# Performance work log

Measured on AMD Instinct MI355X. Metric: run time of the kernel, lower is better.

The kernel has to match this reference:

```python
import jax, jax.numpy as jnp
import numpy as np

N = 12288
E = 393216
D_IN, D_HID, D_OUT = 128, 128, 64


def gcn_conv(x, edge_index, W, b, num_nodes):
    # PyG GCNConv: h = x @ W; add self-loops; sym-normalize; scatter-add; + b
    h = x @ W  # [N, F]
    row, col = edge_index[0], edge_index[1]
    sl = jnp.arange(num_nodes, dtype=edge_index.dtype)
    row = jnp.concatenate([row, sl])
    col = jnp.concatenate([col, sl])
    deg = jax.ops.segment_sum(jnp.ones_like(col, dtype=h.dtype), col, num_segments=num_nodes)
    dinv = jax.lax.rsqrt(jnp.maximum(deg, 1e-12))
    norm = dinv[row] * dinv[col]  # [E+N]
    msgs = h[row] * norm[:, None]
    out = jax.ops.segment_sum(msgs, col, num_segments=num_nodes)
    return out + b


def setup_inputs() -> dict:
    key = jax.random.key(0)
    k1, k2, k3, k4, k5 = jax.random.split(key, 5)
    x = jax.random.uniform(k1, (N, D_IN), dtype=jnp.float32)
    edge_index = jax.random.randint(k2, (2, E), 0, N, dtype=jnp.int64)
    # Glorot-style init for GCN weights, zeros for biases (PyG defaults)
    W1 = jax.random.normal(k3, (D_IN, D_HID), dtype=jnp.float32) * (1.0 / np.sqrt(D_IN))
    b1 = jnp.zeros((D_HID,), dtype=jnp.float32)
    W2 = jax.random.normal(k4, (D_HID, D_OUT), dtype=jnp.float32) * (1.0 / np.sqrt(D_HID))
    b2 = jnp.zeros((D_OUT,), dtype=jnp.float32)
    return {"x": x, "edge_index": edge_index, "W1": W1, "b1": b1, "W2": W2, "b2": b2}


def reference(x, edge_index, W1, b1, W2, b2):
    h = jax.nn.relu(gcn_conv(x, edge_index, W1, b1, N))
    latent = gcn_conv(h, edge_index, W2, b2, N)  # [N, D_OUT]
    return latent @ latent.T  # [N, N] gram-matrix decoder
```

## Files before the change

### kernel.cpp

```cpp
#include <hip/hip_runtime.h>

#define NN   12288
#define EE   393216
#define DIN  128
#define DHID 128
#define DOUT 64
#define CAP  96

typedef __attribute__((ext_vector_type(8))) short bf16x8;
typedef __attribute__((ext_vector_type(4))) float f32x4;
typedef __attribute__((ext_vector_type(4))) short s16x4;

__device__ __forceinline__ short f2bf(float f) {
    unsigned u = __float_as_uint(f);
    unsigned r = (u + 0x7fffu + ((u >> 16) & 1u)) >> 16;
    return (short)r;
}
__device__ __forceinline__ float bf2f(short h) {
    return __uint_as_float(((unsigned)(unsigned short)h) << 16);
}

#define GEMM1_BLOCKS 768
#define FILL_BLOCKS  512
__global__ __launch_bounds__(256) void k_fill_gemm1(const float* __restrict__ x,
                                                    const int* __restrict__ row,
                                                    const int* __restrict__ col,
                                                    const float* __restrict__ W1,
                                                    unsigned* __restrict__ cursor,
                                                    int* __restrict__ bucket,
                                                    float* __restrict__ g1) {
    const int b = blockIdx.x, t = threadIdx.x;
    if (b < GEMM1_BLOCKS) {
        __shared__ float xs[16 * DIN];
        const int r0 = b * 16;
        for (int j = t; j < 16 * DIN; j += 256) xs[j] = x[(size_t)r0 * DIN + j];
        __syncthreads();
        const int c = t & 127, rg = (t >> 7) * 8;
        float acc[8] = {};
        for (int k = 0; k < DIN; ++k) {
            float w = W1[k * DHID + c];
#pragma unroll
            for (int r = 0; r < 8; ++r) acc[r] += xs[(rg + r) * DIN + k] * w;
        }
#pragma unroll
        for (int r = 0; r < 8; ++r) g1[(size_t)(r0 + rg + r) * DHID + c] = acc[r];
    } else {
        const int gid = (b - GEMM1_BLOCKS) * 256 + t;
#pragma unroll
        for (int q = 0; q < 3; ++q) {
            int e = gid + q * (FILL_BLOCKS * 256);
            int c = col[e];
            unsigned p = atomicAdd(&cursor[c], 1u);
            if (p < CAP) bucket[(size_t)c * CAP + p] = row[e];
        }
    }
}

__global__ __launch_bounds__(256) void k_gather1_gemm2(const float* __restrict__ g1,
                                                       const int* __restrict__ bucket,
                                                       const unsigned* __restrict__ cursor,
                                                       const float* __restrict__ b1,
                                                       const float* __restrict__ W2,
                                                       float* __restrict__ g2) {
    __shared__ float hs[4][DHID];
    const int lane = threadIdx.x & 63, wave = threadIdx.x >> 6;
    const int c = blockIdx.x * 4 + wave;
    const unsigned cnt = cursor[c];
    const float dc = rsqrtf((float)cnt + 1.0f);
    const unsigned e = cnt < CAP ? cnt : CAP;
    const f32x4* __restrict__ G4 = (const f32x4*)g1;
    const int* __restrict__ bk = bucket + (size_t)c * CAP;
    const int sub = lane >> 5, col4 = lane & 31;

    f32x4 acc = (f32x4){0.f, 0.f, 0.f, 0.f};
    if (sub == 0) acc = G4[(size_t)c * 32 + col4] * dc;

    unsigned i = 0;
    int pr[4];
    if (i + 8 <= e) {
#pragma unroll
        for (int p = 0; p < 4; ++p) pr[p] = bk[i + 2 * p + sub];
    }
    for (; i + 8 <= e;) {
        int r[4];
#pragma unroll
        for (int p = 0; p < 4; ++p) r[p] = pr[p];
        const unsigned ni = i + 8;
        if (ni + 8 <= e) {
#pragma unroll
            for (int p = 0; p < 4; ++p) pr[p] = bk[ni + 2 * p + sub];
        }
        float d[4];
        f32x4 v[4];
#pragma unroll
        for (int p = 0; p < 4; ++p) {
            d[p] = rsqrtf((float)cursor[r[p]] + 1.0f);
            v[p] = G4[(size_t)r[p] * 32 + col4];
        }
#pragma unroll
        for (int p = 0; p < 4; ++p) acc += v[p] * d[p];
        i = ni;
    }
    for (; i + 2 <= e; i += 2) {
        int rr = bk[i + sub];
        float d = rsqrtf((float)cursor[rr] + 1.0f);
        acc += G4[(size_t)rr * 32 + col4] * d;
    }
    if (i < e && sub == 0) {
        int rr = bk[i];
        float d = rsqrtf((float)cursor[rr] + 1.0f);
        acc += G4[(size_t)rr * 32 + col4] * d;
    }
    acc.x += __shfl_xor(acc.x, 32);
    acc.y += __shfl_xor(acc.y, 32);
    acc.z += __shfl_xor(acc.z, 32);
    acc.w += __shfl_xor(acc.w, 32);

    f32x4 bb = ((const f32x4*)b1)[col4];
    f32x4 o = acc * dc + bb;
    o.x = fmaxf(o.x, 0.f);
    o.y = fmaxf(o.y, 0.f);
    o.z = fmaxf(o.z, 0.f);
    o.w = fmaxf(o.w, 0.f);
    if (sub == 0) ((f32x4*)hs[wave])[col4] = o;

    float a2 = 0.f;
#pragma unroll 8
    for (int k = 0; k < DHID; ++k) a2 += hs[wave][k] * W2[k * DOUT + lane];
    g2[(size_t)c * DOUT + lane] = a2 * dc;
}

__global__ __launch_bounds__(256) void k_gather2(const float* __restrict__ g2,
                                                 const int* __restrict__ bucket,
                                                 const unsigned* __restrict__ cursor,
                                                 const float* __restrict__ b2,
                                                 short* __restrict__ H,
                                                 short* __restrict__ Lo) {
    const int lane = threadIdx.x & 63, wave = threadIdx.x >> 6;
    const int c = blockIdx.x * 4 + wave;
    const unsigned cnt = cursor[c];
    const float dc = rsqrtf((float)cnt + 1.0f);
    const unsigned e = cnt < CAP ? cnt : CAP;
    const f32x4* __restrict__ G4 = (const f32x4*)g2;
    const int* __restrict__ bk = bucket + (size_t)c * CAP;
    const int sub = lane >> 4, col4 = lane & 15;

    f32x4 acc = (f32x4){0.f, 0.f, 0.f, 0.f};
    if (sub == 0) acc = G4[(size_t)c * 16 + col4];

    unsigned i = 0;
    int pr0 = 0, pr1 = 0;
    if (i + 8 <= e) { pr0 = bk[i + sub]; pr1 = bk[i + 4 + sub]; }
    for (; i + 8 <= e;) {
        int r0 = pr0, r1 = pr1;
        const unsigned ni = i + 8;
        if (ni + 8 <= e) { pr0 = bk[ni + sub]; pr1 = bk[ni + 4 + sub]; }
        f32x4 v0 = G4[(size_t)r0 * 16 + col4];
        f32x4 v1 = G4[(size_t)r1 * 16 + col4];
        acc += v0;
        acc += v1;
        i = ni;
    }
    for (; i + 4 <= e; i += 4) {
        int rr = bk[i + sub];
        acc += G4[(size_t)rr * 16 + col4];
    }
    if (i < e) {
        if (sub < (int)(e - i)) {
            int rr = bk[i + sub];
            acc += G4[(size_t)rr * 16 + col4];
        }
    }
    acc.x += __shfl_xor(acc.x, 16); acc.x += __shfl_xor(acc.x, 32);
    acc.y += __shfl_xor(acc.y, 16); acc.y += __shfl_xor(acc.y, 32);
    acc.z += __shfl_xor(acc.z, 16); acc.z += __shfl_xor(acc.z, 32);
    acc.w += __shfl_xor(acc.w, 16); acc.w += __shfl_xor(acc.w, 32);

    if (sub == 0) {
        f32x4 bb = ((const f32x4*)b2)[col4];
        f32x4 v = acc * dc + bb;
        s16x4 h4, l4;
        h4.x = f2bf(v.x); l4.x = f2bf(v.x - bf2f(h4.x));
        h4.y = f2bf(v.y); l4.y = f2bf(v.y - bf2f(h4.y));
        h4.z = f2bf(v.z); l4.z = f2bf(v.z - bf2f(h4.z));
        h4.w = f2bf(v.w); l4.w = f2bf(v.w - bf2f(h4.w));
        ((s16x4*)H)[(size_t)c * 16 + col4] = h4;
        ((s16x4*)Lo)[(size_t)c * 16 + col4] = l4;
    }
}

#define NTILE 96
#define NPAIR ((NTILE * (NTILE + 1)) / 2)
__global__ __launch_bounds__(256) void k_gram(const short* __restrict__ H,
                                              const short* __restrict__ L,
                                              float* __restrict__ out) {
    __shared__ float P[64][132];
    const int tid  = threadIdx.x;
    const int lane = tid & 63;
    const int wave = tid >> 6;

    const int Lb = blockIdx.x;
    int bi = (int)((193.0f - sqrtf(193.0f * 193.0f - 8.0f * (float)Lb)) * 0.5f);
    if (bi < 0) bi = 0;
    if (bi > NTILE - 1) bi = NTILE - 1;
    while (bi * NTILE - (bi * (bi - 1)) / 2 > Lb) --bi;
    while ((bi + 1) * NTILE - ((bi + 1) * bi) / 2 <= Lb) ++bi;
    const int bj = bi + (Lb - (bi * NTILE - (bi * (bi - 1)) / 2));

    const int wm = wave >> 1, wn = wave & 1;
    const int row0 = bi * 128 + wm * 64;
    const int col0 = bj * 128 + wn * 64;
    const int fr = lane & 15;
    const int fk = (lane >> 4) << 3;
    const int crow = (lane >> 4) * 4;
    const bool mirror = (bi != bj);

    bf16x8 aH[4][2], aL[4][2];
#pragma unroll
    for (int m = 0; m < 4; ++m)
#pragma unroll
        for (int k = 0; k < 2; ++k) {
            size_t off = (size_t)(row0 + m * 16 + fr) * DOUT + k * 32 + fk;
            aH[m][k] = *(const bf16x8*)(H + off);
            aL[m][k] = *(const bf16x8*)(L + off);
        }

    f32x4 acc[4][4];
#pragma unroll
    for (int n = 0; n < 4; ++n)
#pragma unroll
        for (int m = 0; m < 4; ++m) acc[n][m] = (f32x4){0.f, 0.f, 0.f, 0.f};

#pragma unroll
    for (int n = 0; n < 4; ++n) {
        bf16x8 bH[2], bL[2];
#pragma unroll
        for (int k = 0; k < 2; ++k) {
            size_t off = (size_t)(col0 + n * 16 + fr) * DOUT + k * 32 + fk;
            bH[k] = *(const bf16x8*)(H + off);
            bL[k] = *(const bf16x8*)(L + off);
        }
#pragma unroll
        for (int m = 0; m < 4; ++m)
#pragma unroll
            for (int k = 0; k < 2; ++k) {
                acc[n][m] = __builtin_amdgcn_mfma_f32_16x16x32_bf16(aL[m][k], bH[k], acc[n][m], 0, 0, 0);
                acc[n][m] = __builtin_amdgcn_mfma_f32_16x16x32_bf16(aH[m][k], bL[k], acc[n][m], 0, 0, 0);
                acc[n][m] = __builtin_amdgcn_mfma_f32_16x16x32_bf16(aH[m][k], bH[k], acc[n][m], 0, 0, 0);
            }
    }

    const size_t gr0 = (size_t)bi * 128, gc0 = (size_t)bj * 128;
#pragma unroll
    for (int h = 0; h < 2; ++h) {
        __syncthreads();
        if (wm == h) {
#pragma unroll
            for (int n = 0; n < 4; ++n)
#pragma unroll
                for (int m = 0; m < 4; ++m)
#pragma unroll
                    for (int j = 0; j < 4; ++j)
                        P[m * 16 + crow + j][wn * 64 + n * 16 + fr] = acc[n][m][j];
        }
        __syncthreads();
#pragma unroll
        for (int it = 0; it < 8; ++it) {
            int idx = it * 256 + tid;
            int r = idx >> 5, c4 = (idx & 31) << 2;
            f32x4 v = *(const f32x4*)&P[r][c4];
            __builtin_nontemporal_store(v, (f32x4*)&out[(gr0 + h * 64 + r) * NN + gc0 + c4]);
        }
        if (mirror) {
#pragma unroll
            for (int it = 0; it < 8; ++it) {
                int idx = it * 256 + tid;
                int r = idx >> 4, c4 = (idx & 15) << 2;
                f32x4 v;
                v.x = P[c4 + 0][r];
                v.y = P[c4 + 1][r];
                v.z = P[c4 + 2][r];
                v.w = P[c4 + 3][r];
                __builtin_nontemporal_store(v, (f32x4*)&out[(gc0 + r) * NN + gr0 + h * 64 + c4]);
            }
        }
    }
}

extern "C" void kernel_launch(void* const* d_in, const int* in_sizes, int n_in,
                              void* d_out, int out_size, void* d_ws, size_t ws_size,
                              hipStream_t stream) {
    const float* x  = (const float*)d_in[0];
    const int*   ei = (const int*)d_in[1];
    const float* W1 = (const float*)d_in[2];
    const float* b1 = (const float*)d_in[3];
    const float* W2 = (const float*)d_in[4];
    const float* b2 = (const float*)d_in[5];
    float* out = (float*)d_out;

    const int* row = ei;
    const int* col = ei + EE;

    char* w = (char*)d_ws;
    unsigned* cursor = (unsigned*)w; w += (size_t)NN * 4;
    int*      bucket = (int*)w;      w += (size_t)NN * CAP * 4;
    float*    g1     = (float*)w;    w += (size_t)NN * DHID * 4;
    float*    g2     = (float*)w;    w += (size_t)NN * DOUT * 4;
    short*    latH   = (short*)w;    w += (size_t)NN * DOUT * 2;
    short*    latL   = (short*)w;    w += (size_t)NN * DOUT * 2;

    hipMemsetAsync(cursor, 0, (size_t)NN * 4, stream);

    k_fill_gemm1<<<GEMM1_BLOCKS + FILL_BLOCKS, 256, 0, stream>>>(x, row, col, W1, cursor, bucket, g1);
    k_gather1_gemm2<<<NN / 4, 256, 0, stream>>>(g1, bucket, cursor, b1, W2, g2);
    k_gather2<<<NN / 4, 256, 0, stream>>>(g2, bucket, cursor, b2, latH, latL);

    k_gram<<<NPAIR, 256, 0, stream>>>(latH, latL, out);
}
```

Measured before the change: 207.9 us.

## Fuse memset, fill/GEMM1, gather1 and gather2 into one cooperative kernel

Replaces the memset plus three separate kernel launches with a single cooperative persistent kernel of 768 blocks that uses grid.sync between phases (cursor clear, bucket fill and GEMM1, gather1+GEMM2, gather2). Per-node gather code is factored into device helpers shared by the fallback kernels. The aim is to remove launch overhead and inter-kernel gaps. In exchange, the grid-wide barriers cost time, each block now serially handles 16 nodes per gather phase with lower occupancy, and the old kernels remain only as a fallback if the cooperative launch fails.

```diff
diff --git a/kernel.cpp b/kernel.cpp
--- a/kernel.cpp
+++ b/kernel.cpp
@@ -1,4 +1,7 @@
 #include <hip/hip_runtime.h>
+#include <hip/hip_cooperative_groups.h>
+
+namespace cg = cooperative_groups;
 
 #define NN   12288
 #define EE   393216
@@ -6,6 +9,7 @@
 #define DHID 128
 #define DOUT 64
 #define CAP  96
+#define NBC  768
 
 typedef __attribute__((ext_vector_type(8))) short bf16x8;
 typedef __attribute__((ext_vector_type(4))) float f32x4;
@@ -18,6 +22,190 @@
 }
 __device__ __forceinline__ float bf2f(short h) {
     return __uint_as_float(((unsigned)(unsigned short)h) << 16);
+}
+
+__device__ __forceinline__ void gather1_gemm2_node(int c, const float* __restrict__ g1,
+                                                   const int* __restrict__ bucket,
+                                                   const unsigned* __restrict__ cursor,
+                                                   const float* __restrict__ b1,
+                                                   const float* __restrict__ W2,
+                                                   float* __restrict__ g2,
+                                                   float* __restrict__ hrow,
+                                                   int lane) {
+    const unsigned cnt = cursor[c];
+    const float dc = rsqrtf((float)cnt + 1.0f);
+    const unsigned e = cnt < CAP ? cnt : CAP;
+    const f32x4* __restrict__ G4 = (const f32x4*)g1;
+    const int* __restrict__ bk = bucket + (size_t)c * CAP;
+    const int sub = lane >> 5, col4 = lane & 31;
+
+    f32x4 acc = (f32x4){0.f, 0.f, 0.f, 0.f};
+    if (sub == 0) acc = G4[(size_t)c * 32 + col4] * dc;
+
+    unsigned i = 0;
+    int pr[4];
+    if (i + 8 <= e) {
+#pragma unroll
+        for (int p = 0; p < 4; ++p) pr[p] = bk[i + 2 * p + sub];
+    }
+    for (; i + 8 <= e;) {
+        int r[4];
+#pragma unroll
+        for (int p = 0; p < 4; ++p) r[p] = pr[p];
+        const unsigned ni = i + 8;
+        if (ni + 8 <= e) {
+#pragma unroll
+            for (int p = 0; p < 4; ++p) pr[p] = bk[ni + 2 * p + sub];
+        }
+        float d[4];
+        f32x4 v[4];
+#pragma unroll
+        for (int p = 0; p < 4; ++p) {
+            d[p] = rsqrtf((float)cursor[r[p]] + 1.0f);
+            v[p] = G4[(size_t)r[p] * 32 + col4];
+        }
+#pragma unroll
+        for (int p = 0; p < 4; ++p) acc += v[p] * d[p];
+        i = ni;
+    }
+    for (; i + 2 <= e; i += 2) {
+        int rr = bk[i + sub];
+        float d = rsqrtf((float)cursor[rr] + 1.0f);
+        acc += G4[(size_t)rr * 32 + col4] * d;
+    }
+    if (i < e && sub == 0) {
+        int rr = bk[i];
+        float d = rsqrtf((float)cursor[rr] + 1.0f);
+        acc += G4[(size_t)rr * 32 + col4] * d;
+    }
+    acc.x += __shfl_xor(acc.x, 32);
+    acc.y += __shfl_xor(acc.y, 32);
+    acc.z += __shfl_xor(acc.z, 32);
+    acc.w += __shfl_xor(acc.w, 32);
+
+    f32x4 bb = ((const f32x4*)b1)[col4];
+    f32x4 o = acc * dc + bb;
+    o.x = fmaxf(o.x, 0.f);
+    o.y = fmaxf(o.y, 0.f);
+    o.z = fmaxf(o.z, 0.f);
+    o.w = fmaxf(o.w, 0.f);
+    if (sub == 0) ((f32x4*)hrow)[col4] = o;
+
+    float a2 = 0.f;
+#pragma unroll 8
+    for (int k = 0; k < DHID; ++k) a2 += hrow[k] * W2[k * DOUT + lane];
+    g2[(size_t)c * DOUT + lane] = a2 * dc;
+}
+
+__device__ __forceinline__ void gather2_node(int c, const float* __restrict__ g2,
+                                             const int* __restrict__ bucket,
+                                             const unsigned* __restrict__ cursor,
+                                             const float* __restrict__ b2,
+                                             short* __restrict__ H, short* __restrict__ Lo,
+                                             int lane) {
+    const unsigned cnt = cursor[c];
+    const float dc = rsqrtf((float)cnt + 1.0f);
+    const unsigned e = cnt < CAP ? cnt : CAP;
+    const f32x4* __restrict__ G4 = (const f32x4*)g2;
+    const int* __restrict__ bk = bucket + (size_t)c * CAP;
+    const int sub = lane >> 4, col4 = lane & 15;
+
+    f32x4 acc = (f32x4){0.f, 0.f, 0.f, 0.f};
+    if (sub == 0) acc = G4[(size_t)c * 16 + col4];
+
+    unsigned i = 0;
+    int pr0 = 0, pr1 = 0;
+    if (i + 8 <= e) { pr0 = bk[i + sub]; pr1 = bk[i + 4 + sub]; }
+    for (; i + 8 <= e;) {
+        int r0 = pr0, r1 = pr1;
+        const unsigned ni = i + 8;
+        if (ni + 8 <= e) { pr0 = bk[ni + sub]; pr1 = bk[ni + 4 + sub]; }
+        f32x4 v0 = G4[(size_t)r0 * 16 + col4];
+        f32x4 v1 = G4[(size_t)r1 * 16 + col4];
+        acc += v0;
+        acc += v1;
+        i = ni;
+    }
+    for (; i + 4 <= e; i += 4) {
+        int rr = bk[i + sub];
+        acc += G4[(size_t)rr * 16 + col4];
+    }
+    if (i < e) {
+        if (sub < (int)(e - i)) {
+            int rr = bk[i + sub];
+            acc += G4[(size_t)rr * 16 + col4];
+        }
+    }
+    acc.x += __shfl_xor(acc.x, 16); acc.x += __shfl_xor(acc.x, 32);
+    acc.y += __shfl_xor(acc.y, 16); acc.y += __shfl_xor(acc.y, 32);
+    acc.z += __shfl_xor(acc.z, 16); acc.z += __shfl_xor(acc.z, 32);
+    acc.w += __shfl_xor(acc.w, 16); acc.w += __shfl_xor(acc.w, 32);
+
+    if (sub == 0) {
+        f32x4 bb = ((const f32x4*)b2)[col4];
+        f32x4 v = acc * dc + bb;
+        s16x4 h4, l4;
+        h4.x = f2bf(v.x); l4.x = f2bf(v.x - bf2f(h4.x));
+        h4.y = f2bf(v.y); l4.y = f2bf(v.y - bf2f(h4.y));
+        h4.z = f2bf(v.z); l4.z = f2bf(v.z - bf2f(h4.z));
+        h4.w = f2bf(v.w); l4.w = f2bf(v.w - bf2f(h4.w));
+        ((s16x4*)H)[(size_t)c * 16 + col4] = h4;
+        ((s16x4*)Lo)[(size_t)c * 16 + col4] = l4;
+    }
+}
+
+__global__ __launch_bounds__(256, 3) void k_mega(
+    const float* __restrict__ x, const int* __restrict__ row, const int* __restrict__ col,
+    const float* __restrict__ W1, const float* __restrict__ b1,
+    const float* __restrict__ W2, const float* __restrict__ b2,
+    unsigned* __restrict__ cursor, int* __restrict__ bucket,
+    float* __restrict__ g1, float* __restrict__ g2,
+    short* __restrict__ latH, short* __restrict__ latL) {
+    cg::grid_group grid = cg::this_grid();
+    const int t = threadIdx.x, b = blockIdx.x;
+    const int gid = b * 256 + t;
+    const int lane = t & 63, wave = t >> 6;
+
+    __shared__ float smem[16 * DIN];
+
+    if (gid < NN) cursor[gid] = 0;
+    grid.sync();
+
+    {
+        int e0 = gid, e1 = gid + NBC * 256;
+        int c0 = col[e0], c1 = col[e1];
+        unsigned p0 = atomicAdd(&cursor[c0], 1u);
+        unsigned p1 = atomicAdd(&cursor[c1], 1u);
+        if (p0 < CAP) bucket[(size_t)c0 * CAP + p0] = row[e0];
+        if (p1 < CAP) bucket[(size_t)c1 * CAP + p1] = row[e1];
+    }
+    {
+        const int r0 = b * 16;
+        for (int j = t; j < 16 * DIN; j += 256) smem[j] = x[(size_t)r0 * DIN + j];
+        __syncthreads();
+        const int c = t & 127, rg = (t >> 7) * 8;
+        float acc[8] = {};
+        for (int k = 0; k < DIN; ++k) {
+            float w = W1[k * DHID + c];
+#pragma unroll
+            for (int r = 0; r < 8; ++r) acc[r] += smem[(rg + r) * DIN + k] * w;
+        }
+#pragma unroll
+        for (int r = 0; r < 8; ++r) g1[(size_t)(r0 + rg + r) * DHID + c] = acc[r];
+    }
+    grid.sync();
+
+    {
+        float* hrow = &smem[wave * DHID];
+#pragma unroll
+        for (int it = 0; it < 4; ++it)
+            gather1_gemm2_node(b * 16 + it * 4 + wave, g1, bucket, cursor, b1, W2, g2, hrow, lane);
+    }
+    grid.sync();
+
+#pragma unroll
+    for (int it = 0; it < 4; ++it)
+        gather2_node(b * 16 + it * 4 + wave, g2, bucket, cursor, b2, latH, latL, lane);
 }
 
 #define GEMM1_BLOCKS 768
@@ -64,70 +252,7 @@
                                                        float* __restrict__ g2) {
     __shared__ float hs[4][DHID];
     const int lane = threadIdx.x & 63, wave = threadIdx.x >> 6;
-    const int c = blockIdx.x * 4 + wave;
-    const unsigned cnt = cursor[c];
-    const float dc = rsqrtf((float)cnt + 1.0f);
-    const unsigned e = cnt < CAP ? cnt : CAP;
-    const f32x4* __restrict__ G4 = (const f32x4*)g1;
-    const int* __restrict__ bk = bucket + (size_t)c * CAP;
-    const int sub = lane >> 5, col4 = lane & 31;
-
-    f32x4 acc = (f32x4){0.f, 0.f, 0.f, 0.f};
-    if (sub == 0) acc = G4[(size_t)c * 32 + col4] * dc;
-
-    unsigned i = 0;
-    int pr[4];
-    if (i + 8 <= e) {
-#pragma unroll
-        for (int p = 0; p < 4; ++p) pr[p] = bk[i + 2 * p + sub];
-    }
-    for (; i + 8 <= e;) {
-        int r[4];
-#pragma unroll
-        for (int p = 0; p < 4; ++p) r[p] = pr[p];
-        const unsigned ni = i + 8;
-        if (ni + 8 <= e) {
-#pragma unroll
-            for (int p = 0; p < 4; ++p) pr[p] = bk[ni + 2 * p + sub];
-        }
-        float d[4];
-        f32x4 v[4];
-#pragma unroll
-        for (int p = 0; p < 4; ++p) {
-            d[p] = rsqrtf((float)cursor[r[p]] + 1.0f);
-            v[p] = G4[(size_t)r[p] * 32 + col4];
-        }
-#pragma unroll
-        for (int p = 0; p < 4; ++p) acc += v[p] * d[p];
-        i = ni;
-    }
-    for (; i + 2 <= e; i += 2) {
-        int rr = bk[i + sub];
-        float d = rsqrtf((float)cursor[rr] + 1.0f);
-        acc += G4[(size_t)rr * 32 + col4] * d;
-    }
-    if (i < e && sub == 0) {
-        int rr = bk[i];
-        float d = rsqrtf((float)cursor[rr] + 1.0f);
-        acc += G4[(size_t)rr * 32 + col4] * d;
-    }
-    acc.x += __shfl_xor(acc.x, 32);
-    acc.y += __shfl_xor(acc.y, 32);
-    acc.z += __shfl_xor(acc.z, 32);
-    acc.w += __shfl_xor(acc.w, 32);
-
-    f32x4 bb = ((const f32x4*)b1)[col4];
-    f32x4 o = acc * dc + bb;
-    o.x = fmaxf(o.x, 0.f);
-    o.y = fmaxf(o.y, 0.f);
-    o.z = fmaxf(o.z, 0.f);
-    o.w = fmaxf(o.w, 0.f);
-    if (sub == 0) ((f32x4*)hs[wave])[col4] = o;
-
-    float a2 = 0.f;
-#pragma unroll 8
-    for (int k = 0; k < DHID; ++k) a2 += hs[wave][k] * W2[k * DOUT + lane];
-    g2[(size_t)c * DOUT + lane] = a2 * dc;
+    gather1_gemm2_node(blockIdx.x * 4 + wave, g1, bucket, cursor, b1, W2, g2, hs[wave], lane);
 }
 
 __global__ __launch_bounds__(256) void k_gather2(const float* __restrict__ g2,
@@ -137,56 +262,7 @@
                                                  short* __restrict__ H,
                                                  short* __restrict__ Lo) {
     const int lane = threadIdx.x & 63, wave = threadIdx.x >> 6;
-    const int c = blockIdx.x * 4 + wave;
-    const unsigned cnt = cursor[c];
-    const float dc = rsqrtf((float)cnt + 1.0f);
-    const unsigned e = cnt < CAP ? cnt : CAP;
-    const f32x4* __restrict__ G4 = (const f32x4*)g2;
-    const int* __restrict__ bk = bucket + (size_t)c * CAP;
-    const int sub = lane >> 4, col4 = lane & 15;
-
-    f32x4 acc = (f32x4){0.f, 0.f, 0.f, 0.f};
-    if (sub == 0) acc = G4[(size_t)c * 16 + col4];
-
-    unsigned i = 0;
-    int pr0 = 0, pr1 = 0;
-    if (i + 8 <= e) { pr0 = bk[i + sub]; pr1 = bk[i + 4 + sub]; }
-    for (; i + 8 <= e;) {
-        int r0 = pr0, r1 = pr1;
-        const unsigned ni = i + 8;
-        if (ni + 8 <= e) { pr0 = bk[ni + sub]; pr1 = bk[ni + 4 + sub]; }
-        f32x4 v0 = G4[(size_t)r0 * 16 + col4];
-        f32x4 v1 = G4[(size_t)r1 * 16 + col4];
-        acc += v0;
-        acc += v1;
-        i = ni;
-    }
-    for (; i + 4 <= e; i += 4) {
-        int rr = bk[i + sub];
-        acc += G4[(size_t)rr * 16 + col4];
-    }
-    if (i < e) {
-        if (sub < (int)(e - i)) {
-            int rr = bk[i + sub];
-            acc += G4[(size_t)rr * 16 + col4];
-        }
-    }
-    acc.x += __shfl_xor(acc.x, 16); acc.x += __shfl_xor(acc.x, 32);
-    acc.y += __shfl_xor(acc.y, 16); acc.y += __shfl_xor(acc.y, 32);
-    acc.z += __shfl_xor(acc.z, 16); acc.z += __shfl_xor(acc.z, 32);
-    acc.w += __shfl_xor(acc.w, 16); acc.w += __shfl_xor(acc.w, 32);
-
-    if (sub == 0) {
-        f32x4 bb = ((const f32x4*)b2)[col4];
-        f32x4 v = acc * dc + bb;
-        s16x4 h4, l4;
-        h4.x = f2bf(v.x); l4.x = f2bf(v.x - bf2f(h4.x));
-        h4.y = f2bf(v.y); l4.y = f2bf(v.y - bf2f(h4.y));
-        h4.z = f2bf(v.z); l4.z = f2bf(v.z - bf2f(h4.z));
-        h4.w = f2bf(v.w); l4.w = f2bf(v.w - bf2f(h4.w));
-        ((s16x4*)H)[(size_t)c * 16 + col4] = h4;
-        ((s16x4*)Lo)[(size_t)c * 16 + col4] = l4;
-    }
+    gather2_node(blockIdx.x * 4 + wave, g2, bucket, cursor, b2, H, Lo, lane);
 }
 
 #define NTILE 96
@@ -309,11 +385,18 @@
     short*    latH   = (short*)w;    w += (size_t)NN * DOUT * 2;
     short*    latL   = (short*)w;    w += (size_t)NN * DOUT * 2;
 
-    hipMemsetAsync(cursor, 0, (size_t)NN * 4, stream);
-
-    k_fill_gemm1<<<GEMM1_BLOCKS + FILL_BLOCKS, 256, 0, stream>>>(x, row, col, W1, cursor, bucket, g1);
-    k_gather1_gemm2<<<NN / 4, 256, 0, stream>>>(g1, bucket, cursor, b1, W2, g2);
-    k_gather2<<<NN / 4, 256, 0, stream>>>(g2, bucket, cursor, b2, latH, latL);
+    void* args[] = {(void*)&x, (void*)&row, (void*)&col, (void*)&W1, (void*)&b1,
+                    (void*)&W2, (void*)&b2, (void*)&cursor, (void*)&bucket,
+                    (void*)&g1, (void*)&g2, (void*)&latH, (void*)&latL};
+    hipError_t err = hipLaunchCooperativeKernel((const void*)k_mega, dim3(NBC), dim3(256),
+                                                args, 0, stream);
+    if (err != hipSuccess) {
+        (void)hipGetLastError();
+        hipMemsetAsync(cursor, 0, (size_t)NN * 4, stream);
+        k_fill_gemm1<<<GEMM1_BLOCKS + FILL_BLOCKS, 256, 0, stream>>>(x, row, col, W1, cursor, bucket, g1);
+        k_gather1_gemm2<<<NN / 4, 256, 0, stream>>>(g1, bucket, cursor, b1, W2, g2);
+        k_gather2<<<NN / 4, 256, 0, stream>>>(g2, bucket, cursor, b2, latH, latL);
+    }
 
     k_gram<<<NPAIR, 256, 0, stream>>>(latH, latL, out);
 }
```

New measurement: 451.2 us. 117% more time.
